# Performance work log

Hardware: AMD Instinct MI355X
Metric: run time of the kernel (lower is better)

## Reference

```python
import jax, jax.numpy as jnp
import numpy as np

DIM = 512
HEADS = 8
WIN = 64


def setup_inputs() -> dict:
    key = jax.random.key(0)
    k1, k2, k3 = jax.random.split(key, 3)
    x = jax.random.normal(k1, (16, 4096, DIM), dtype=jnp.float32)
    Wqkv = jax.random.normal(k2, (DIM, 3 * DIM), dtype=jnp.float32) * 0.02
    Wproj = jax.random.normal(k3, (DIM, DIM), dtype=jnp.float32) * 0.02
    bproj = jnp.zeros((DIM,), dtype=jnp.float32)
    return {"x": x, "Wqkv": Wqkv, "Wproj": Wproj, "bproj": bproj}


def reference(x, Wqkv, Wproj, bproj):
    B0, T0, C = x.shape
    H = HEADS
    hd = C // H
    scale = hd ** -0.5
    # reshape sequence into fixed-size windows: [Bw, W, C]
    xw = x.reshape(-1, WIN, C)
    Bw = xw.shape[0]
    # fused QKV projection (no bias)
    qkv = (xw @ Wqkv).reshape(Bw, WIN, 3, H, hd)
    qkv = jnp.transpose(qkv, (2, 0, 3, 1, 4))  # [3, Bw, H, W, hd]
    q, k, v = qkv[0], qkv[1], qkv[2]
    attn = jnp.einsum('bhqd,bhkd->bhqk', q, k) * scale  # [Bw, H, W, W]
    # causal mask within each window
    mask = jnp.tril(jnp.ones((WIN, WIN), dtype=bool))
    attn = jnp.where(mask, attn, -jnp.inf)
    attn = jax.nn.softmax(attn, axis=-1)
    # faithful to source: second (unconditional) softmax applied on probabilities
    attn = jax.nn.softmax(attn, axis=-1)
    out = jnp.einsum('bhqk,bhkd->bhqd', attn, v)  # [Bw, H, W, hd]
    out = jnp.transpose(out, (0, 2, 1, 3)).reshape(Bw, WIN, C)
    out = out @ Wproj + bproj
    return out.reshape(B0, T0, C)
```

## Files before the change

### kernel.cpp

```cpp
#include <hip/hip_runtime.h>


typedef _Float16 f16x8 __attribute__((ext_vector_type(8)));
typedef _Float16 f16x4 __attribute__((ext_vector_type(4)));
typedef float f32x4 __attribute__((ext_vector_type(4)));

#define MFMA16(a, b, c) __builtin_amdgcn_mfma_f32_16x16x32_f16((a), (b), (c), 0, 0, 0)

__device__ __forceinline__ int swz64(int r, int c) { return r * 64 + (c ^ ((r & 7) << 3)); }
__device__ __forceinline__ int swz512(int r, int c) { return r * 512 + (c ^ ((r & 7) << 3)); }

typedef const __attribute__((address_space(1))) void* gas1_t;
typedef __attribute__((address_space(3))) void* las3_t;

__device__ __forceinline__ void stage16(const _Float16* g, _Float16* lbase, int lane) {
#if __has_builtin(__builtin_amdgcn_global_load_lds)
  __builtin_amdgcn_global_load_lds((gas1_t)(const void*)g, (las3_t)(void*)lbase, 16, 0, 0);
#else
  *(f16x8*)(lbase + lane * 8) = *(const f16x8*)g;
#endif
}

__global__ void prep_weights(const float* __restrict__ Wqkv,
                             const float* __restrict__ Wproj,
                             _Float16* __restrict__ wqkvP,
                             _Float16* __restrict__ wprojP) {
  int idx = blockIdx.x * blockDim.x + threadIdx.x;
  if (idx < 786432) {
    int r16 = idx >> 13;
    int rem = idx & 8191;
    int kt = rem >> 9;
    int lane = (rem >> 3) & 63;
    int e = rem & 7;
    int row = r16 * 16 + (lane & 15);
    int k = kt * 32 + (lane >> 4) * 8 + e;
    float v = Wqkv[k * 1536 + row];
    if (row < 512) v *= 0.125f;
    wqkvP[idx] = (_Float16)v;
  } else {
    int j = idx - 786432;
    int r16 = j >> 13;
    int rem = j & 8191;
    int kt = rem >> 9;
    int lane = (rem >> 3) & 63;
    int e = rem & 7;
    int n = r16 * 16 + (lane & 15);
    int k = kt * 32 + (lane >> 4) * 8 + e;
    wprojP[j] = (_Float16)Wproj[k * 512 + n];
  }
}

__global__ __launch_bounds__(512) void prep_x(const float* __restrict__ x,
                                              _Float16* __restrict__ xP) {
  __shared__ __align__(16) _Float16 sX[64 * 512];
  const int tid = threadIdx.x;
  const float4* xv = (const float4*)(x + (size_t)blockIdx.x * 32768);
#pragma unroll
  for (int it = 0; it < 8; ++it) {
    int g = tid + it * 512;
    int r = g >> 6, c0 = (g & 63) << 3;
    float4 a = xv[(r << 7) + (c0 >> 2)];
    float4 b = xv[(r << 7) + (c0 >> 2) + 1];
    f16x8 hv;
    hv[0] = (_Float16)a.x; hv[1] = (_Float16)a.y;
    hv[2] = (_Float16)a.z; hv[3] = (_Float16)a.w;
    hv[4] = (_Float16)b.x; hv[5] = (_Float16)b.y;
    hv[6] = (_Float16)b.z; hv[7] = (_Float16)b.w;
    *(f16x8*)&sX[swz512(r, c0)] = hv;
  }
  __syncthreads();
  _Float16* dst = xP + (size_t)blockIdx.x * 32768;
#pragma unroll
  for (int it = 0; it < 8; ++it) {
    int c8 = tid + it * 512;
    int rt = c8 >> 10, ks = (c8 >> 6) & 15, ln = c8 & 63;
    int row = rt * 16 + (ln & 15);
    int k0 = ks * 32 + (ln >> 4) * 8;
    f16x8 v = *(const f16x8*)&sX[swz512(row, k0)];
    *(f16x8*)(dst + c8 * 8) = v;
  }
}

template <int MODE>
__global__ __launch_bounds__(512, 2) void gemm2p(
    const _Float16* __restrict__ Afp, const _Float16* __restrict__ Bfp,
    _Float16* __restrict__ dst16, float* __restrict__ out,
    const float* __restrict__ bproj, int rTiles) {
  __shared__ __align__(16) _Float16 sG[2][2][16][512];
  const int tid = threadIdx.x;
  const int wid = tid >> 6;
  const int lane = tid & 63;
  const int lg = lane >> 4, lr = lane & 15;
  const int wr = wid >> 2, wc = wid & 3;
  const int wr8 = wr * 8, wc4 = wc * 4, lane8 = lane * 8;

  const int nwg = gridDim.x;
  const int bid = blockIdx.x;
  const int swz = (bid & 7) * (nwg >> 3) + (bid >> 3);
  const int r0 = (swz % rTiles) * 256, c0 = (swz / rTiles) * 256;

  const _Float16* Abase = Afp + (size_t)(r0 >> 4) * 8192 + lane8;
  const _Float16* Bbase = Bfp + (size_t)(c0 >> 4) * 8192 + lane8;

  const f32x4 zero4 = {0.f, 0.f, 0.f, 0.f};
  f32x4 acc[8][4];
#pragma unroll
  for (int i = 0; i < 8; ++i)
#pragma unroll
    for (int j = 0; j < 4; ++j) acc[i][j] = zero4;

  const int cs = wid * 2;
  auto STAGE = [&](int s, int T) {
    stage16(Abase + (size_t)cs * 8192 + T * 512, &sG[s][0][cs][0], lane);
    stage16(Abase + (size_t)(cs + 1) * 8192 + T * 512, &sG[s][0][cs + 1][0], lane);
    stage16(Bbase + (size_t)cs * 8192 + T * 512, &sG[s][1][cs][0], lane);
    stage16(Bbase + (size_t)(cs + 1) * 8192 + T * 512, &sG[s][1][cs + 1][0], lane);
  };

  STAGE(0, 0);
  int cur = 0;
  for (int t = 0; t < 16; ++t) {
    const int Tn = (t + 1 < 16) ? t + 1 : 15;
    STAGE(cur ^ 1, Tn);
    asm volatile("s_waitcnt vmcnt(4)");
    __builtin_amdgcn_s_barrier();
    __builtin_amdgcn_sched_barrier(0);
    f16x8 a[8], b[4];
#pragma unroll
    for (int mi = 0; mi < 8; ++mi)
      a[mi] = *(const f16x8*)&sG[cur][0][wr8 + mi][lane8];
#pragma unroll
    for (int ni = 0; ni < 4; ++ni)
      b[ni] = *(const f16x8*)&sG[cur][1][wc4 + ni][lane8];
    __builtin_amdgcn_s_setprio(1);
#pragma unroll
    for (int mi = 0; mi < 8; ++mi)
#pragma unroll
      for (int ni = 0; ni < 4; ++ni)
        acc[mi][ni] = MFMA16(a[mi], b[ni], acc[mi][ni]);
    __builtin_amdgcn_s_setprio(0);
    asm volatile("s_waitcnt lgkmcnt(0)");
    __builtin_amdgcn_sched_barrier(0);
    __builtin_amdgcn_s_barrier();
    __builtin_amdgcn_sched_barrier(0);
    cur ^= 1;
  }

  if constexpr (MODE == 0) {
#pragma unroll
    for (int mi = 0; mi < 8; ++mi) {
      int nb = r0 + wr * 128 + mi * 16 + lg * 4;
      int sec = nb >> 9, h = (nb >> 6) & 7, db = nb & 63;
      int coff = (db >> 5) * 512 + (((db >> 3) & 3) * 16) * 8 + (db & 7);
#pragma unroll
      for (int ni = 0; ni < 4; ++ni) {
        int tg = c0 + wc * 64 + ni * 16 + lr;
        int w = tg >> 6, t = tg & 63;
        size_t pos = ((size_t)w * 24 + sec * 8 + h) * 4096 +
                     (size_t)((t >> 4) * 2) * 512 + coff + (t & 15) * 8;
        f16x4 hv;
        hv[0] = (_Float16)acc[mi][ni][0]; hv[1] = (_Float16)acc[mi][ni][1];
        hv[2] = (_Float16)acc[mi][ni][2]; hv[3] = (_Float16)acc[mi][ni][3];
        *(f16x4*)(dst16 + pos) = hv;
      }
    }
  } else if constexpr (MODE == 1) {
#pragma unroll
    for (int mi = 0; mi < 8; ++mi) {
      int tbg = r0 + wr * 128 + mi * 16 + lg * 4;
      int w = tbg >> 6, tb = tbg & 63;
      int coff = (tb >> 5) * 512 + (((tb >> 3) & 3) * 16) * 8 + (tb & 7);
#pragma unroll
      for (int ni = 0; ni < 4; ++ni) {
        int cv = c0 + wc * 64 + ni * 16 + lr;
        int h = cv >> 6, d = cv & 63;
        size_t pos = ((size_t)w * 24 + 16 + h) * 4096 +
                     (size_t)((d >> 4) * 2) * 512 + coff + (d & 15) * 8;
        f16x4 hv;
        hv[0] = (_Float16)acc[mi][ni][0]; hv[1] = (_Float16)acc[mi][ni][1];
        hv[2] = (_Float16)acc[mi][ni][2]; hv[3] = (_Float16)acc[mi][ni][3];
        *(f16x4*)(dst16 + pos) = hv;
      }
    }
  } else {
#pragma unroll
    for (int mi = 0; mi < 8; ++mi) {
      int nb = r0 + wr * 128 + mi * 16 + lg * 4;
      float4 bi = *(const float4*)&bproj[nb];
#pragma unroll
      for (int ni = 0; ni < 4; ++ni) {
        int tg = c0 + wc * 64 + ni * 16 + lr;
        float4 v;
        v.x = acc[mi][ni][0] + bi.x; v.y = acc[mi][ni][1] + bi.y;
        v.z = acc[mi][ni][2] + bi.z; v.w = acc[mi][ni][3] + bi.w;
        *(float4*)&out[(size_t)tg * 512 + nb] = v;
      }
    }
  }
}

__global__ __launch_bounds__(512, 4) void attn_win(
    const _Float16* __restrict__ qkvP, _Float16* __restrict__ hP) {
  __shared__ __align__(16) _Float16 sP[4][4096];
  const int tid = threadIdx.x;
  const int wid = tid >> 6;
  const int lane = tid & 63;
  const int lg = lane >> 4, lr = lane & 15;
  const int hl = wid >> 1, part = wid & 1;
  const int w = blockIdx.x;
  const f32x4 zero4 = {0.f, 0.f, 0.f, 0.f};

  for (int hr = 0; hr < 2; ++hr) {
    const int h = hr * 4 + hl;
    const _Float16* Qb = qkvP + ((size_t)w * 24 + h) * 4096 + lane * 8;
    const _Float16* Kb = qkvP + ((size_t)w * 24 + 8 + h) * 4096 + lane * 8;
    const _Float16* Vb = qkvP + ((size_t)w * 24 + 16 + h) * 4096 + lane * 8;

    f16x8 afq[2][2], bfk[4][2];
#pragma unroll
    for (int rs = 0; rs < 2; ++rs)
#pragma unroll
      for (int dkt = 0; dkt < 2; ++dkt)
        afq[rs][dkt] = *(const f16x8*)(Qb + ((part * 2 + rs) * 2 + dkt) * 512);
#pragma unroll
    for (int nt = 0; nt < 4; ++nt)
#pragma unroll
      for (int dkt = 0; dkt < 2; ++dkt)
        bfk[nt][dkt] = *(const f16x8*)(Kb + (nt * 2 + dkt) * 512);
    f32x4 sacc[2][4];
#pragma unroll
    for (int rs = 0; rs < 2; ++rs)
#pragma unroll
      for (int nt = 0; nt < 4; ++nt) sacc[rs][nt] = zero4;
#pragma unroll
    for (int dkt = 0; dkt < 2; ++dkt)
#pragma unroll
      for (int rs = 0; rs < 2; ++rs)
#pragma unroll
        for (int nt = 0; nt < 4; ++nt)
          sacc[rs][nt] = MFMA16(afq[rs][dkt], bfk[nt][dkt], sacc[rs][nt]);

    f16x8 afv[2][2];
#pragma unroll
    for (int ds = 0; ds < 2; ++ds)
#pragma unroll
      for (int tkt = 0; tkt < 2; ++tkt)
        afv[ds][tkt] = *(const f16x8*)(Vb + ((part * 2 + ds) * 2 + tkt) * 512);

    float p2[2][4][4];
#pragma unroll
    for (int rs = 0; rs < 2; ++rs) {
      const int rsg = part * 2 + rs;
#pragma unroll
      for (int rg = 0; rg < 4; ++rg) {
        int row = rsg * 16 + lg * 4 + rg;
        float m = -1e30f;
#pragma unroll
        for (int nt = 0; nt < 4; ++nt) {
          int col = nt * 16 + lr;
          float v = (col <= row) ? sacc[rs][nt][rg] : -1e30f;
          m = fmaxf(m, v);
        }
#pragma unroll
        for (int off = 8; off >= 1; off >>= 1) m = fmaxf(m, __shfl_xor(m, off));
        float e[4], s1 = 0.f;
#pragma unroll
        for (int nt = 0; nt < 4; ++nt) {
          int col = nt * 16 + lr;
          e[nt] = (col <= row) ? __expf(sacc[rs][nt][rg] - m) : 0.f;
          s1 += e[nt];
        }
#pragma unroll
        for (int off = 8; off >= 1; off >>= 1) s1 += __shfl_xor(s1, off);
        float inv1 = 1.f / s1;
        float e2[4], s2 = 0.f;
#pragma unroll
        for (int nt = 0; nt < 4; ++nt) {
          e2[nt] = __expf(e[nt] * inv1);
          s2 += e2[nt];
        }
#pragma unroll
        for (int off = 8; off >= 1; off >>= 1) s2 += __shfl_xor(s2, off);
        float inv2 = 1.f / s2;
#pragma unroll
        for (int nt = 0; nt < 4; ++nt) p2[rs][nt][rg] = e2[nt] * inv2;
      }
    }

#pragma unroll
    for (int rs = 0; rs < 2; ++rs) {
      const int rsg = part * 2 + rs;
#pragma unroll
      for (int nt = 0; nt < 4; ++nt) {
        int cbase = (rsg * 2 + (nt >> 1)) * 512 +
                    ((((nt * 2) + (lr >> 3)) & 3) * 16 + lg * 4) * 8 + (lr & 7);
#pragma unroll
        for (int rg = 0; rg < 4; ++rg)
          sP[hl][cbase + rg * 8] = (_Float16)p2[rs][nt][rg];
      }
    }
    __syncthreads();

    f32x4 oacc[2][4];
#pragma unroll
    for (int ds = 0; ds < 2; ++ds)
#pragma unroll
      for (int ntq = 0; ntq < 4; ++ntq) oacc[ds][ntq] = zero4;
#pragma unroll
    for (int tkt = 0; tkt < 2; ++tkt) {
      f16x8 bfp[4];
#pragma unroll
      for (int ntq = 0; ntq < 4; ++ntq)
        bfp[ntq] = *(const f16x8*)&sP[hl][(ntq * 2 + tkt) * 512 + lane * 8];
#pragma unroll
      for (int ds = 0; ds < 2; ++ds)
#pragma unroll
        for (int ntq = 0; ntq < 4; ++ntq)
          oacc[ds][ntq] = MFMA16(afv[ds][tkt], bfp[ntq], oacc[ds][ntq]);
    }

#pragma unroll
    for (int ds = 0; ds < 2; ++ds) {
      const int dsg = part * 2 + ds;
      const int e0 = (lg & 1) * 4;
      const int lgt = (dsg * 2 + (lg >> 1)) & 3;
#pragma unroll
      for (int ntq = 0; ntq < 4; ++ntq) {
        size_t pos = ((size_t)(w * 4 + ntq) * 16 + h * 2 + (dsg >> 1)) * 512 +
                     (lgt * 16 + lr) * 8 + e0;
        f16x4 hv;
        hv[0] = (_Float16)oacc[ds][ntq][0]; hv[1] = (_Float16)oacc[ds][ntq][1];
        hv[2] = (_Float16)oacc[ds][ntq][2]; hv[3] = (_Float16)oacc[ds][ntq][3];
        *(f16x4*)(hP + pos) = hv;
      }
    }
    __syncthreads();
  }
}

__global__ __launch_bounds__(512, 2) void attn_fused(
    const float* __restrict__ x, const _Float16* __restrict__ wqkvP,
    const _Float16* __restrict__ wprojP, const float* __restrict__ bproj,
    float* __restrict__ out) {
  __shared__ __align__(16) _Float16 sX[64 * 512];
  __shared__ __align__(16) _Float16 sHeads[4][2][4096];

  const int tid = threadIdx.x;
  const int wid = tid >> 6;
  const int lane = tid & 63;
  const int lg = lane >> 4;
  const int lr = lane & 15;

  _Float16* sQ0 = &sHeads[0][0][0];
  _Float16* sK0 = &sHeads[1][0][0];
  _Float16* sVT0 = &sHeads[2][0][0];
  _Float16* sPO0 = &sHeads[3][0][0];

  const float4* xv = (const float4*)(x + (size_t)blockIdx.x * 32768);
#pragma unroll
  for (int it = 0; it < 8; ++it) {
    int g = tid + it * 512;
    int r = g >> 6, c0 = (g & 63) << 3;
    float4 a = xv[(r << 7) + (c0 >> 2)];
    float4 b = xv[(r << 7) + (c0 >> 2) + 1];
    f16x8 hv;
    hv[0] = (_Float16)a.x; hv[1] = (_Float16)a.y;
    hv[2] = (_Float16)a.z; hv[3] = (_Float16)a.w;
    hv[4] = (_Float16)b.x; hv[5] = (_Float16)b.y;
    hv[6] = (_Float16)b.z; hv[7] = (_Float16)b.w;
    *(f16x8*)&sX[swz512(r, c0)] = hv;
  }
  const f32x4 zero4 = {0.f, 0.f, 0.f, 0.f};
  f32x4 accO[4][4];
#pragma unroll
  for (int i = 0; i < 4; ++i)
#pragma unroll
    for (int j = 0; j < 4; ++j) accO[i][j] = zero4;
  __syncthreads();

  for (int hp = 0; hp < 4; ++hp) {
    int hu[3], su[3], stu[3];
    const _Float16* bp[3];
    f32x4 acc[3][4];
#pragma unroll
    for (int i = 0; i < 3; ++i) {
      int u = wid + 8 * i;
      int hh = u & 1, v2 = u >> 1;
      int sec = v2 % 3, strip = v2 / 3;
      hu[i] = hh; su[i] = sec; stu[i] = strip;
      int r16 = sec * 32 + (hp * 2 + hh) * 4 + strip;
      bp[i] = wqkvP + (size_t)r16 * 8192 + lane * 8;
#pragma unroll
      for (int rt = 0; rt < 4; ++rt) acc[i][rt] = zero4;
    }
    f16x8 bf[3][3];
#pragma unroll
    for (int d = 0; d < 3; ++d)
#pragma unroll
      for (int i = 0; i < 3; ++i) bf[d][i] = *(const f16x8*)(bp[i] + d * 512);
    f16x8 af[2][4];
#pragma unroll
    for (int rt = 0; rt < 4; ++rt)
      af[0][rt] = *(const f16x8*)&sX[swz512(rt * 16 + lr, lg * 8)];
#pragma unroll
    for (int ks = 0; ks < 16; ++ks) {
      if (ks < 15) {
#pragma unroll
        for (int rt = 0; rt < 4; ++rt)
          af[(ks + 1) & 1][rt] =
              *(const f16x8*)&sX[swz512(rt * 16 + lr, (ks + 1) * 32 + lg * 8)];
      }
#pragma unroll
      for (int i = 0; i < 3; ++i)
#pragma unroll
        for (int rt = 0; rt < 4; ++rt)
          acc[i][rt] = MFMA16(af[ks & 1][rt], bf[ks % 3][i], acc[i][rt]);
      if (ks + 3 < 16) {
#pragma unroll
        for (int i = 0; i < 3; ++i)
          bf[ks % 3][i] = *(const f16x8*)(bp[i] + (ks + 3) * 512);
      }
    }
#pragma unroll
    for (int i = 0; i < 3; ++i) {
      int hh = hu[i], sec = su[i], strip = stu[i];
      _Float16* dq = sQ0 + hh * 4096;
      _Float16* dk = sK0 + hh * 4096;
      _Float16* dv = sVT0 + hh * 4096;
#pragma unroll
      for (int rt = 0; rt < 4; ++rt)
#pragma unroll
        for (int rg = 0; rg < 4; ++rg) {
          int row = rt * 16 + lg * 4 + rg;
          int col = strip * 16 + lr;
          _Float16 v = (_Float16)acc[i][rt][rg];
          if (sec == 0) dq[swz64(row, col)] = v;
          else if (sec == 1) dk[swz64(row, col)] = v;
          else dv[swz64(col, row)] = v;
        }
    }
    __syncthreads();
    {
      const int hh = wid >> 2;
      const int rs = wid & 3;
      const _Float16* mQ = sQ0 + hh * 4096;
      const _Float16* mK = sK0 + hh * 4096;
      const _Float16* mV = sVT0 + hh * 4096;
      _Float16* mP = sPO0 + hh * 4096;
      f32x4 sacc[4];
#pragma unroll
      for (int nt = 0; nt < 4; ++nt) sacc[nt] = zero4;
#pragma unroll
      for (int ks = 0; ks < 2; ++ks) {
        f16x8 afq = *(const f16x8*)&mQ[swz64(rs * 16 + lr, ks * 32 + lg * 8)];
#pragma unroll
        for (int nt = 0; nt < 4; ++nt) {
          f16x8 bfk = *(const f16x8*)&mK[swz64(nt * 16 + lr, ks * 32 + lg * 8)];
          sacc[nt] = MFMA16(afq, bfk, sacc[nt]);
        }
      }
      float p2[4][4];
#pragma unroll
      for (int rg = 0; rg < 4; ++rg) {
        int row = rs * 16 + lg * 4 + rg;
        float m = -1e30f;
#pragma unroll
        for (int nt = 0; nt < 4; ++nt) {
          int col = nt * 16 + lr;
          float v = (col <= row) ? sacc[nt][rg] : -1e30f;
          m = fmaxf(m, v);
        }
#pragma unroll
        for (int off = 8; off >= 1; off >>= 1) m = fmaxf(m, __shfl_xor(m, off));
        float e[4], s1 = 0.f;
#pragma unroll
        for (int nt = 0; nt < 4; ++nt) {
          int col = nt * 16 + lr;
          e[nt] = (col <= row) ? __expf(sacc[nt][rg] - m) : 0.f;
          s1 += e[nt];
        }
#pragma unroll
        for (int off = 8; off >= 1; off >>= 1) s1 += __shfl_xor(s1, off);
        float inv1 = 1.f / s1;
        float e2[4], s2 = 0.f;
#pragma unroll
        for (int nt = 0; nt < 4; ++nt) {
          e2[nt] = __expf(e[nt] * inv1);
          s2 += e2[nt];
        }
#pragma unroll
        for (int off = 8; off >= 1; off >>= 1) s2 += __shfl_xor(s2, off);
        float inv2 = 1.f / s2;
#pragma unroll
        for (int nt = 0; nt < 4; ++nt) p2[nt][rg] = e2[nt] * inv2;
      }
#pragma unroll
      for (int nt = 0; nt < 4; ++nt)
#pragma unroll
        for (int rg = 0; rg < 4; ++rg)
          mP[swz64(rs * 16 + lg * 4 + rg, nt * 16 + lr)] = (_Float16)p2[nt][rg];
      asm volatile("" ::: "memory");
      f32x4 oacc[4];
#pragma unroll
      for (int nt = 0; nt < 4; ++nt) oacc[nt] = zero4;
#pragma unroll
      for (int ks = 0; ks < 2; ++ks) {
        f16x8 afp = *(const f16x8*)&mP[swz64(rs * 16 + lr, ks * 32 + lg * 8)];
#pragma unroll
        for (int nt = 0; nt < 4; ++nt) {
          f16x8 bfv = *(const f16x8*)&mV[swz64(nt * 16 + lr, ks * 32 + lg * 8)];
          oacc[nt] = MFMA16(afp, bfv, oacc[nt]);
        }
      }
      asm volatile("" ::: "memory");
#pragma unroll
      for (int nt = 0; nt < 4; ++nt)
#pragma unroll
        for (int rg = 0; rg < 4; ++rg)
          mP[swz64(rs * 16 + lg * 4 + rg, nt * 16 + lr)] = (_Float16)oacc[nt][rg];
    }
    __syncthreads();
    {
      f16x8 bfC[2][4], afC[2][4];
#pragma unroll
      for (int rt = 0; rt < 4; ++rt)
        afC[0][rt] = *(const f16x8*)&sPO0[swz64(rt * 16 + lr, lg * 8)];
#pragma unroll
      for (int nt = 0; nt < 4; ++nt)
        bfC[0][nt] = *(const f16x8*)(wprojP + (size_t)(wid * 4 + nt) * 8192 +
                                     (size_t)(hp * 4) * 512 + lane * 8);
#pragma unroll
      for (int g = 0; g < 4; ++g) {
        if (g < 3) {
          int hn = (g + 1) >> 1, kn = (g + 1) & 1;
#pragma unroll
          for (int rt = 0; rt < 4; ++rt)
            afC[(g + 1) & 1][rt] = *(const f16x8*)&sPO0[hn * 4096 +
                swz64(rt * 16 + lr, kn * 32 + lg * 8)];
#pragma unroll
          for (int nt = 0; nt < 4; ++nt)
            bfC[(g + 1) & 1][nt] =
                *(const f16x8*)(wprojP + (size_t)(wid * 4 + nt) * 8192 +
                                (size_t)(hp * 4 + g + 1) * 512 + lane * 8);
        }
#pragma unroll
        for (int nt = 0; nt < 4; ++nt)
#pragma unroll
          for (int rt = 0; rt < 4; ++rt)
            accO[rt][nt] = MFMA16(afC[g & 1][rt], bfC[g & 1][nt], accO[rt][nt]);
      }
    }
  }
  __syncthreads();
  float bias_r[4];
#pragma unroll
  for (int nt = 0; nt < 4; ++nt) bias_r[nt] = bproj[wid * 64 + nt * 16 + lr];
  float* sEp = (float*)&sHeads[0][0][0];
  size_t base = (size_t)blockIdx.x * 32768;
#pragma unroll
  for (int half = 0; half < 2; ++half) {
#pragma unroll
    for (int rr = 0; rr < 2; ++rr) {
      int rt = half * 2 + rr;
#pragma unroll
      for (int nt = 0; nt < 4; ++nt)
#pragma unroll
        for (int rg = 0; rg < 4; ++rg) {
          int r = rr * 16 + lg * 4 + rg;
          int c = wid * 64 + nt * 16 + lr;
          sEp[r * 512 + (c ^ (((r >> 2) & 1) << 4))] = accO[rt][nt][rg] + bias_r[nt];
        }
    }
    __syncthreads();
#pragma unroll
    for (int j = 0; j < 8; ++j) {
      int f4 = tid + j * 512;
      int r = f4 >> 7;
      int c0 = (f4 & 127) << 2;
      float4 v = *(const float4*)&sEp[r * 512 + (c0 ^ (((r >> 2) & 1) << 4))];
      *(float4*)&out[base + (size_t)(half * 32 + r) * 512 + c0] = v;
    }
    if (half == 0) __syncthreads();
  }
}

extern "C" void kernel_launch(void* const* d_in, const int* in_sizes, int n_in,
                              void* d_out, int out_size, void* d_ws, size_t ws_size,
                              hipStream_t stream) {
  const float* x = (const float*)d_in[0];
  const float* Wqkv = (const float*)d_in[1];
  const float* Wproj = (const float*)d_in[2];
  const float* bproj = (const float*)d_in[3];
  float* out = (float*)d_out;

  const size_t W1 = 786432, W2 = 262144, XN = 33554432;
  const size_t QN = 100663296, HN = 33554432;
  _Float16* wqkvP = (_Float16*)d_ws;
  _Float16* wprojP = wqkvP + W1;
  _Float16* xP = wprojP + W2;
  _Float16* qkvP = xP + XN;
  _Float16* hP = qkvP + QN;
  const size_t NEED = (W1 + W2 + XN + QN + HN) * 2;

  prep_weights<<<dim3(4096), dim3(256), 0, stream>>>(Wqkv, Wproj, wqkvP, wprojP);
  if (ws_size >= NEED) {
    prep_x<<<dim3(1024), dim3(512), 0, stream>>>(x, xP);
    gemm2p<0><<<dim3(1024), dim3(512), 0, stream>>>(wqkvP, xP, qkvP, nullptr, nullptr, 4);
    gemm2p<1><<<dim3(512), dim3(512), 0, stream>>>(xP, wqkvP + (size_t)64 * 8192,
                                                   qkvP, nullptr, nullptr, 256);
    attn_win<<<dim3(1024), dim3(512), 0, stream>>>(qkvP, hP);
    gemm2p<2><<<dim3(512), dim3(512), 0, stream>>>(wprojP, hP, nullptr, out, bproj, 2);
  } else {
    attn_fused<<<dim3(1024), dim3(512), 0, stream>>>(x, wqkvP, wprojP, bproj, out);
  }
}
```

Before: 294.2 us.

## Load GEMM B fragments directly into registers, stage only A through LDS

The GEMM kernel no longer stages the B operand in shared memory. Each wave loads its own B fragments straight from global memory into double-buffered registers, while A keeps LDS double buffering. This halves LDS use and the LDS traffic for B. In exchange, B fragments shared across wave rows are now fetched redundantly from global/L2, register pressure rises, and the loop is fully unrolled.

```diff
diff --git a/kernel.cpp b/kernel.cpp
--- a/kernel.cpp
+++ b/kernel.cpp
@@ -7,8 +7,8 @@
 
 #define MFMA16(a, b, c) __builtin_amdgcn_mfma_f32_16x16x32_f16((a), (b), (c), 0, 0, 0)
 
+__device__ __forceinline__ int swz512(int r, int c) { return r * 512 + (c ^ ((r & 7) << 3)); }
 __device__ __forceinline__ int swz64(int r, int c) { return r * 64 + (c ^ ((r & 7) << 3)); }
-__device__ __forceinline__ int swz512(int r, int c) { return r * 512 + (c ^ ((r & 7) << 3)); }
 
 typedef const __attribute__((address_space(1))) void* gas1_t;
 typedef __attribute__((address_space(3))) void* las3_t;
@@ -82,17 +82,18 @@
 }
 
 template <int MODE>
-__global__ __launch_bounds__(512, 2) void gemm2p(
+__global__ __launch_bounds__(512, 2) void gemmd(
     const _Float16* __restrict__ Afp, const _Float16* __restrict__ Bfp,
     _Float16* __restrict__ dst16, float* __restrict__ out,
     const float* __restrict__ bproj, int rTiles) {
-  __shared__ __align__(16) _Float16 sG[2][2][16][512];
+  __shared__ __align__(16) _Float16 sA[2][16][512];
   const int tid = threadIdx.x;
   const int wid = tid >> 6;
   const int lane = tid & 63;
   const int lg = lane >> 4, lr = lane & 15;
   const int wr = wid >> 2, wc = wid & 3;
   const int wr8 = wr * 8, wc4 = wc * 4, lane8 = lane * 8;
+  const int cs = wid * 2;
 
   const int nwg = gridDim.x;
   const int bid = blockIdx.x;
@@ -100,7 +101,12 @@
   const int r0 = (swz % rTiles) * 256, c0 = (swz / rTiles) * 256;
 
   const _Float16* Abase = Afp + (size_t)(r0 >> 4) * 8192 + lane8;
-  const _Float16* Bbase = Bfp + (size_t)(c0 >> 4) * 8192 + lane8;
+  const _Float16* Bfrag = Bfp + (size_t)((c0 >> 4) + wc4) * 8192 + lane8;
+
+  auto ASTAGE = [&](int s, int T) {
+    stage16(Abase + (size_t)cs * 8192 + T * 512, &sA[s][cs][0], lane);
+    stage16(Abase + (size_t)(cs + 1) * 8192 + T * 512, &sA[s][cs + 1][0], lane);
+  };
 
   const f32x4 zero4 = {0.f, 0.f, 0.f, 0.f};
   f32x4 acc[8][4];
@@ -109,41 +115,53 @@
 #pragma unroll
     for (int j = 0; j < 4; ++j) acc[i][j] = zero4;
 
-  const int cs = wid * 2;
-  auto STAGE = [&](int s, int T) {
-    stage16(Abase + (size_t)cs * 8192 + T * 512, &sG[s][0][cs][0], lane);
-    stage16(Abase + (size_t)(cs + 1) * 8192 + T * 512, &sG[s][0][cs + 1][0], lane);
-    stage16(Bbase + (size_t)cs * 8192 + T * 512, &sG[s][1][cs][0], lane);
-    stage16(Bbase + (size_t)(cs + 1) * 8192 + T * 512, &sG[s][1][cs + 1][0], lane);
-  };
-
-  STAGE(0, 0);
-  int cur = 0;
+  f16x8 bA[4], bB[4];
+#pragma unroll
+  for (int ni = 0; ni < 4; ++ni)
+    bA[ni] = *(const f16x8*)(Bfrag + (size_t)ni * 8192);
+  ASTAGE(0, 0);
+
+#pragma unroll
   for (int t = 0; t < 16; ++t) {
+    const int s = t & 1, sn = s ^ 1;
     const int Tn = (t + 1 < 16) ? t + 1 : 15;
-    STAGE(cur ^ 1, Tn);
-    asm volatile("s_waitcnt vmcnt(4)");
+    if ((t & 1) == 0) {
+#pragma unroll
+      for (int ni = 0; ni < 4; ++ni)
+        bB[ni] = *(const f16x8*)(Bfrag + (size_t)ni * 8192 + Tn * 512);
+    } else {
+#pragma unroll
+      for (int ni = 0; ni < 4; ++ni)
+        bA[ni] = *(const f16x8*)(Bfrag + (size_t)ni * 8192 + Tn * 512);
+    }
+    ASTAGE(sn, Tn);
+    __builtin_amdgcn_sched_barrier(0);
+    asm volatile("s_waitcnt vmcnt(6)");
     __builtin_amdgcn_s_barrier();
     __builtin_amdgcn_sched_barrier(0);
-    f16x8 a[8], b[4];
+    f16x8 a[8];
 #pragma unroll
     for (int mi = 0; mi < 8; ++mi)
-      a[mi] = *(const f16x8*)&sG[cur][0][wr8 + mi][lane8];
-#pragma unroll
-    for (int ni = 0; ni < 4; ++ni)
-      b[ni] = *(const f16x8*)&sG[cur][1][wc4 + ni][lane8];
+      a[mi] = *(const f16x8*)&sA[s][wr8 + mi][lane8];
     __builtin_amdgcn_s_setprio(1);
-#pragma unroll
-    for (int mi = 0; mi < 8; ++mi)
-#pragma unroll
-      for (int ni = 0; ni < 4; ++ni)
-        acc[mi][ni] = MFMA16(a[mi], b[ni], acc[mi][ni]);
+    if ((t & 1) == 0) {
+#pragma unroll
+      for (int mi = 0; mi < 8; ++mi)
+#pragma unroll
+        for (int ni = 0; ni < 4; ++ni)
+          acc[mi][ni] = MFMA16(a[mi], bA[ni], acc[mi][ni]);
+    } else {
+#pragma unroll
+      for (int mi = 0; mi < 8; ++mi)
+#pragma unroll
+        for (int ni = 0; ni < 4; ++ni)
+          acc[mi][ni] = MFMA16(a[mi], bB[ni], acc[mi][ni]);
+    }
     __builtin_amdgcn_s_setprio(0);
     asm volatile("s_waitcnt lgkmcnt(0)");
     __builtin_amdgcn_sched_barrier(0);
     __builtin_amdgcn_s_barrier();
     __builtin_amdgcn_sched_barrier(0);
-    cur ^= 1;
   }
 
   if constexpr (MODE == 0) {
@@ -605,11 +623,11 @@
   prep_weights<<<dim3(4096), dim3(256), 0, stream>>>(Wqkv, Wproj, wqkvP, wprojP);
   if (ws_size >= NEED) {
     prep_x<<<dim3(1024), dim3(512), 0, stream>>>(x, xP);
-    gemm2p<0><<<dim3(1024), dim3(512), 0, stream>>>(wqkvP, xP, qkvP, nullptr, nullptr, 4);
-    gemm2p<1><<<dim3(512), dim3(512), 0, stream>>>(xP, wqkvP + (size_t)64 * 8192,
-                                                   qkvP, nullptr, nullptr, 256);
+    gemmd<0><<<dim3(1024), dim3(512), 0, stream>>>(wqkvP, xP, qkvP, nullptr, nullptr, 4);
+    gemmd<1><<<dim3(512), dim3(512), 0, stream>>>(xP, wqkvP + (size_t)64 * 8192,
+                                                  qkvP, nullptr, nullptr, 256);
     attn_win<<<dim3(1024), dim3(512), 0, stream>>>(qkvP, hP);
-    gemm2p<2><<<dim3(512), dim3(512), 0, stream>>>(wprojP, hP, nullptr, out, bproj, 2);
+    gemmd<2><<<dim3(512), dim3(512), 0, stream>>>(wprojP, hP, nullptr, out, bproj, 2);
   } else {
     attn_fused<<<dim3(1024), dim3(512), 0, stream>>>(x, wqkvP, wprojP, bproj, out);
   }
```

Result: slower. 300.6 us (+2.2%).

## Merge QKV GEMMs into one launch and fuse attention with output projection

Applied to the files above, without the earlier changes.

The separate Q/K and V GEMM launches become a single 1536-block GEMM whose epilogue branches by output section and writes V with scalar transposed stores. The attention kernel now also performs the output projection per window: each head pair's output goes to LDS and is multiplied by Wproj fragments read from global memory, accumulating in registers. This removes the intermediate head buffer round trip through HBM and one kernel launch. In exchange, V is written with 2-byte scalar stores, Wproj is reread by every window block, and the attention kernel needs more registers at lower occupancy.

```diff
diff --git a/kernel.cpp b/kernel.cpp
--- a/kernel.cpp
+++ b/kernel.cpp
@@ -7,8 +7,8 @@
 
 #define MFMA16(a, b, c) __builtin_amdgcn_mfma_f32_16x16x32_f16((a), (b), (c), 0, 0, 0)
 
+__device__ __forceinline__ int swz512(int r, int c) { return r * 512 + (c ^ ((r & 7) << 3)); }
 __device__ __forceinline__ int swz64(int r, int c) { return r * 64 + (c ^ ((r & 7) << 3)); }
-__device__ __forceinline__ int swz512(int r, int c) { return r * 512 + (c ^ ((r & 7) << 3)); }
 
 typedef const __attribute__((address_space(1))) void* gas1_t;
 typedef __attribute__((address_space(3))) void* las3_t;
@@ -81,11 +81,9 @@
   }
 }
 
-template <int MODE>
-__global__ __launch_bounds__(512, 2) void gemm2p(
+__global__ __launch_bounds__(512, 2) void gemmQKV(
     const _Float16* __restrict__ Afp, const _Float16* __restrict__ Bfp,
-    _Float16* __restrict__ dst16, float* __restrict__ out,
-    const float* __restrict__ bproj, int rTiles) {
+    _Float16* __restrict__ dst16) {
   __shared__ __align__(16) _Float16 sG[2][2][16][512];
   const int tid = threadIdx.x;
   const int wid = tid >> 6;
@@ -93,29 +91,29 @@
   const int lg = lane >> 4, lr = lane & 15;
   const int wr = wid >> 2, wc = wid & 3;
   const int wr8 = wr * 8, wc4 = wc * 4, lane8 = lane * 8;
+  const int cs = wid * 2;
 
   const int nwg = gridDim.x;
   const int bid = blockIdx.x;
   const int swz = (bid & 7) * (nwg >> 3) + (bid >> 3);
-  const int r0 = (swz % rTiles) * 256, c0 = (swz / rTiles) * 256;
+  const int r0 = (swz % 6) * 256, c0 = (swz / 6) * 256;
 
   const _Float16* Abase = Afp + (size_t)(r0 >> 4) * 8192 + lane8;
   const _Float16* Bbase = Bfp + (size_t)(c0 >> 4) * 8192 + lane8;
 
-  const f32x4 zero4 = {0.f, 0.f, 0.f, 0.f};
-  f32x4 acc[8][4];
-#pragma unroll
-  for (int i = 0; i < 8; ++i)
-#pragma unroll
-    for (int j = 0; j < 4; ++j) acc[i][j] = zero4;
-
-  const int cs = wid * 2;
   auto STAGE = [&](int s, int T) {
     stage16(Abase + (size_t)cs * 8192 + T * 512, &sG[s][0][cs][0], lane);
     stage16(Abase + (size_t)(cs + 1) * 8192 + T * 512, &sG[s][0][cs + 1][0], lane);
     stage16(Bbase + (size_t)cs * 8192 + T * 512, &sG[s][1][cs][0], lane);
     stage16(Bbase + (size_t)(cs + 1) * 8192 + T * 512, &sG[s][1][cs + 1][0], lane);
   };
+
+  const f32x4 zero4 = {0.f, 0.f, 0.f, 0.f};
+  f32x4 acc[8][4];
+#pragma unroll
+  for (int i = 0; i < 8; ++i)
+#pragma unroll
+    for (int j = 0; j < 4; ++j) acc[i][j] = zero4;
 
   STAGE(0, 0);
   int cur = 0;
@@ -146,10 +144,10 @@
     cur ^= 1;
   }
 
-  if constexpr (MODE == 0) {
-#pragma unroll
-    for (int mi = 0; mi < 8; ++mi) {
-      int nb = r0 + wr * 128 + mi * 16 + lg * 4;
+#pragma unroll
+  for (int mi = 0; mi < 8; ++mi) {
+    int nb = r0 + wr * 128 + mi * 16 + lg * 4;
+    if (nb < 1024) {
       int sec = nb >> 9, h = (nb >> 6) & 7, db = nb & 63;
       int coff = (db >> 5) * 512 + (((db >> 3) & 3) * 16) * 8 + (db & 7);
 #pragma unroll
@@ -163,102 +161,71 @@
         hv[2] = (_Float16)acc[mi][ni][2]; hv[3] = (_Float16)acc[mi][ni][3];
         *(f16x4*)(dst16 + pos) = hv;
       }
-    }
-  } else if constexpr (MODE == 1) {
-#pragma unroll
-    for (int mi = 0; mi < 8; ++mi) {
-      int tbg = r0 + wr * 128 + mi * 16 + lg * 4;
-      int w = tbg >> 6, tb = tbg & 63;
-      int coff = (tb >> 5) * 512 + (((tb >> 3) & 3) * 16) * 8 + (tb & 7);
-#pragma unroll
-      for (int ni = 0; ni < 4; ++ni) {
-        int cv = c0 + wc * 64 + ni * 16 + lr;
-        int h = cv >> 6, d = cv & 63;
-        size_t pos = ((size_t)w * 24 + 16 + h) * 4096 +
-                     (size_t)((d >> 4) * 2) * 512 + coff + (d & 15) * 8;
-        f16x4 hv;
-        hv[0] = (_Float16)acc[mi][ni][0]; hv[1] = (_Float16)acc[mi][ni][1];
-        hv[2] = (_Float16)acc[mi][ni][2]; hv[3] = (_Float16)acc[mi][ni][3];
-        *(f16x4*)(dst16 + pos) = hv;
-      }
-    }
-  } else {
-#pragma unroll
-    for (int mi = 0; mi < 8; ++mi) {
-      int nb = r0 + wr * 128 + mi * 16 + lg * 4;
-      float4 bi = *(const float4*)&bproj[nb];
+    } else {
+      int h = (nb >> 6) & 7, db = nb & 63;
 #pragma unroll
       for (int ni = 0; ni < 4; ++ni) {
         int tg = c0 + wc * 64 + ni * 16 + lr;
-        float4 v;
-        v.x = acc[mi][ni][0] + bi.x; v.y = acc[mi][ni][1] + bi.y;
-        v.z = acc[mi][ni][2] + bi.z; v.w = acc[mi][ni][3] + bi.w;
-        *(float4*)&out[(size_t)tg * 512 + nb] = v;
-      }
-    }
-  }
-}
-
-__global__ __launch_bounds__(512, 4) void attn_win(
-    const _Float16* __restrict__ qkvP, _Float16* __restrict__ hP) {
-  __shared__ __align__(16) _Float16 sP[4][4096];
+        int w = tg >> 6, t = tg & 63;
+        size_t base2 = ((size_t)w * 24 + 16 + h) * 4096 +
+                       (size_t)((db >> 4) * 2 + (t >> 5)) * 512 +
+                       (((t >> 3) & 3) * 16) * 8 + (t & 7);
+#pragma unroll
+        for (int rg = 0; rg < 4; ++rg)
+          dst16[base2 + ((db & 15) + rg) * 8] = (_Float16)acc[mi][ni][rg];
+      }
+    }
+  }
+}
+
+__global__ __launch_bounds__(512, 2) void attn_proj(
+    const _Float16* __restrict__ qkvP, const _Float16* __restrict__ wprojP,
+    const float* __restrict__ bproj, float* __restrict__ out) {
+  __shared__ __align__(16) _Float16 sPO[2][4096];
   const int tid = threadIdx.x;
   const int wid = tid >> 6;
   const int lane = tid & 63;
   const int lg = lane >> 4, lr = lane & 15;
-  const int hl = wid >> 1, part = wid & 1;
   const int w = blockIdx.x;
   const f32x4 zero4 = {0.f, 0.f, 0.f, 0.f};
 
-  for (int hr = 0; hr < 2; ++hr) {
-    const int h = hr * 4 + hl;
-    const _Float16* Qb = qkvP + ((size_t)w * 24 + h) * 4096 + lane * 8;
-    const _Float16* Kb = qkvP + ((size_t)w * 24 + 8 + h) * 4096 + lane * 8;
-    const _Float16* Vb = qkvP + ((size_t)w * 24 + 16 + h) * 4096 + lane * 8;
-
-    f16x8 afq[2][2], bfk[4][2];
-#pragma unroll
-    for (int rs = 0; rs < 2; ++rs)
-#pragma unroll
-      for (int dkt = 0; dkt < 2; ++dkt)
-        afq[rs][dkt] = *(const f16x8*)(Qb + ((part * 2 + rs) * 2 + dkt) * 512);
-#pragma unroll
-    for (int nt = 0; nt < 4; ++nt)
-#pragma unroll
-      for (int dkt = 0; dkt < 2; ++dkt)
-        bfk[nt][dkt] = *(const f16x8*)(Kb + (nt * 2 + dkt) * 512);
-    f32x4 sacc[2][4];
-#pragma unroll
-    for (int rs = 0; rs < 2; ++rs)
-#pragma unroll
-      for (int nt = 0; nt < 4; ++nt) sacc[rs][nt] = zero4;
-#pragma unroll
-    for (int dkt = 0; dkt < 2; ++dkt)
-#pragma unroll
-      for (int rs = 0; rs < 2; ++rs)
-#pragma unroll
-        for (int nt = 0; nt < 4; ++nt)
-          sacc[rs][nt] = MFMA16(afq[rs][dkt], bfk[nt][dkt], sacc[rs][nt]);
-
-    f16x8 afv[2][2];
-#pragma unroll
-    for (int ds = 0; ds < 2; ++ds)
-#pragma unroll
-      for (int tkt = 0; tkt < 2; ++tkt)
-        afv[ds][tkt] = *(const f16x8*)(Vb + ((part * 2 + ds) * 2 + tkt) * 512);
-
-    float p2[2][4][4];
-#pragma unroll
-    for (int rs = 0; rs < 2; ++rs) {
-      const int rsg = part * 2 + rs;
+  f32x4 accO[4][4];
+#pragma unroll
+  for (int i = 0; i < 4; ++i)
+#pragma unroll
+    for (int j = 0; j < 4; ++j) accO[i][j] = zero4;
+
+  for (int hp = 0; hp < 4; ++hp) {
+    {
+      const int hh = wid >> 2;
+      const int rs = wid & 3;
+      const int h = hp * 2 + hh;
+      const _Float16* Qb = qkvP + ((size_t)w * 24 + h) * 4096 + lane * 8;
+      const _Float16* Kb = qkvP + ((size_t)w * 24 + 8 + h) * 4096 + lane * 8;
+      const _Float16* Vb = qkvP + ((size_t)w * 24 + 16 + h) * 4096 + lane * 8;
+      _Float16* mP = &sPO[hh][0];
+
+      f32x4 sacc[4];
+#pragma unroll
+      for (int nt = 0; nt < 4; ++nt) sacc[nt] = zero4;
+#pragma unroll
+      for (int dkt = 0; dkt < 2; ++dkt) {
+        f16x8 afq = *(const f16x8*)(Qb + (rs * 2 + dkt) * 512);
+#pragma unroll
+        for (int nt = 0; nt < 4; ++nt) {
+          f16x8 bfk = *(const f16x8*)(Kb + (nt * 2 + dkt) * 512);
+          sacc[nt] = MFMA16(afq, bfk, sacc[nt]);
+        }
+      }
+      float p2[4][4];
 #pragma unroll
       for (int rg = 0; rg < 4; ++rg) {
-        int row = rsg * 16 + lg * 4 + rg;
+        int row = rs * 16 + lg * 4 + rg;
         float m = -1e30f;
 #pragma unroll
         for (int nt = 0; nt < 4; ++nt) {
           int col = nt * 16 + lr;
-          float v = (col <= row) ? sacc[rs][nt][rg] : -1e30f;
+          float v = (col <= row) ? sacc[nt][rg] : -1e30f;
           m = fmaxf(m, v);
         }
 #pragma unroll
@@ -267,7 +234,7 @@
 #pragma unroll
         for (int nt = 0; nt < 4; ++nt) {
           int col = nt * 16 + lr;
-          e[nt] = (col <= row) ? __expf(sacc[rs][nt][rg] - m) : 0.f;
+          e[nt] = (col <= row) ? __expf(sacc[nt][rg] - m) : 0.f;
           s1 += e[nt];
         }
 #pragma unroll
@@ -283,58 +250,66 @@
         for (int off = 8; off >= 1; off >>= 1) s2 += __shfl_xor(s2, off);
         float inv2 = 1.f / s2;
 #pragma unroll
-        for (int nt = 0; nt < 4; ++nt) p2[rs][nt][rg] = e2[nt] * inv2;
-      }
-    }
-
-#pragma unroll
-    for (int rs = 0; rs < 2; ++rs) {
-      const int rsg = part * 2 + rs;
+        for (int nt = 0; nt < 4; ++nt) p2[nt][rg] = e2[nt] * inv2;
+      }
+#pragma unroll
+      for (int nt = 0; nt < 4; ++nt)
+#pragma unroll
+        for (int rg = 0; rg < 4; ++rg)
+          mP[swz64(rs * 16 + lg * 4 + rg, nt * 16 + lr)] = (_Float16)p2[nt][rg];
+      asm volatile("" ::: "memory");
+      f32x4 oacc[4];
+#pragma unroll
+      for (int nt = 0; nt < 4; ++nt) oacc[nt] = zero4;
+#pragma unroll
+      for (int tkt = 0; tkt < 2; ++tkt) {
+        f16x8 afp = *(const f16x8*)&mP[swz64(rs * 16 + lr, tkt * 32 + lg * 8)];
+#pragma unroll
+        for (int nt = 0; nt < 4; ++nt) {
+          f16x8 bfv = *(const f16x8*)(Vb + (nt * 2 + tkt) * 512);
+          oacc[nt] = MFMA16(afp, bfv, oacc[nt]);
+        }
+      }
+      asm volatile("" ::: "memory");
+#pragma unroll
+      for (int nt = 0; nt < 4; ++nt)
+#pragma unroll
+        for (int rg = 0; rg < 4; ++rg)
+          mP[swz64(rs * 16 + lg * 4 + rg, nt * 16 + lr)] = (_Float16)oacc[nt][rg];
+    }
+    __syncthreads();
+
+#pragma unroll
+    for (int ks = 0; ks < 4; ++ks) {
+      const int hh = ks >> 1, d0 = (ks & 1) * 32 + lg * 8;
+      f16x8 bf[4];
+#pragma unroll
+      for (int tt = 0; tt < 4; ++tt)
+        bf[tt] = *(const f16x8*)&sPO[hh][swz64(tt * 16 + lr, d0)];
 #pragma unroll
       for (int nt = 0; nt < 4; ++nt) {
-        int cbase = (rsg * 2 + (nt >> 1)) * 512 +
-                    ((((nt * 2) + (lr >> 3)) & 3) * 16 + lg * 4) * 8 + (lr & 7);
-#pragma unroll
-        for (int rg = 0; rg < 4; ++rg)
-          sP[hl][cbase + rg * 8] = (_Float16)p2[rs][nt][rg];
+        f16x8 aw = *(const f16x8*)(wprojP + (size_t)(wid * 4 + nt) * 8192 +
+                                   (size_t)(hp * 4 + ks) * 512 + lane * 8);
+#pragma unroll
+        for (int tt = 0; tt < 4; ++tt)
+          accO[nt][tt] = MFMA16(aw, bf[tt], accO[nt][tt]);
       }
     }
     __syncthreads();
-
-    f32x4 oacc[2][4];
-#pragma unroll
-    for (int ds = 0; ds < 2; ++ds)
-#pragma unroll
-      for (int ntq = 0; ntq < 4; ++ntq) oacc[ds][ntq] = zero4;
-#pragma unroll
-    for (int tkt = 0; tkt < 2; ++tkt) {
-      f16x8 bfp[4];
-#pragma unroll
-      for (int ntq = 0; ntq < 4; ++ntq)
-        bfp[ntq] = *(const f16x8*)&sP[hl][(ntq * 2 + tkt) * 512 + lane * 8];
-#pragma unroll
-      for (int ds = 0; ds < 2; ++ds)
-#pragma unroll
-        for (int ntq = 0; ntq < 4; ++ntq)
-          oacc[ds][ntq] = MFMA16(afv[ds][tkt], bfp[ntq], oacc[ds][ntq]);
-    }
-
-#pragma unroll
-    for (int ds = 0; ds < 2; ++ds) {
-      const int dsg = part * 2 + ds;
-      const int e0 = (lg & 1) * 4;
-      const int lgt = (dsg * 2 + (lg >> 1)) & 3;
-#pragma unroll
-      for (int ntq = 0; ntq < 4; ++ntq) {
-        size_t pos = ((size_t)(w * 4 + ntq) * 16 + h * 2 + (dsg >> 1)) * 512 +
-                     (lgt * 16 + lr) * 8 + e0;
-        f16x4 hv;
-        hv[0] = (_Float16)oacc[ds][ntq][0]; hv[1] = (_Float16)oacc[ds][ntq][1];
-        hv[2] = (_Float16)oacc[ds][ntq][2]; hv[3] = (_Float16)oacc[ds][ntq][3];
-        *(f16x4*)(hP + pos) = hv;
-      }
-    }
-    __syncthreads();
+  }
+
+#pragma unroll
+  for (int nt = 0; nt < 4; ++nt) {
+    int nb = wid * 64 + nt * 16 + lg * 4;
+    float4 bi = *(const float4*)&bproj[nb];
+#pragma unroll
+    for (int tt = 0; tt < 4; ++tt) {
+      int tok = tt * 16 + lr;
+      float4 v;
+      v.x = accO[nt][tt][0] + bi.x; v.y = accO[nt][tt][1] + bi.y;
+      v.z = accO[nt][tt][2] + bi.z; v.w = accO[nt][tt][3] + bi.w;
+      *(float4*)&out[((size_t)w * 64 + tok) * 512 + nb] = v;
+    }
   }
 }
 
@@ -593,23 +568,18 @@
   const float* bproj = (const float*)d_in[3];
   float* out = (float*)d_out;
 
-  const size_t W1 = 786432, W2 = 262144, XN = 33554432;
-  const size_t QN = 100663296, HN = 33554432;
+  const size_t W1 = 786432, W2 = 262144, XN = 33554432, QN = 100663296;
   _Float16* wqkvP = (_Float16*)d_ws;
   _Float16* wprojP = wqkvP + W1;
   _Float16* xP = wprojP + W2;
   _Float16* qkvP = xP + XN;
-  _Float16* hP = qkvP + QN;
-  const size_t NEED = (W1 + W2 + XN + QN + HN) * 2;
+  const size_t NEED = (W1 + W2 + XN + QN) * 2;
 
   prep_weights<<<dim3(4096), dim3(256), 0, stream>>>(Wqkv, Wproj, wqkvP, wprojP);
   if (ws_size >= NEED) {
     prep_x<<<dim3(1024), dim3(512), 0, stream>>>(x, xP);
-    gemm2p<0><<<dim3(1024), dim3(512), 0, stream>>>(wqkvP, xP, qkvP, nullptr, nullptr, 4);
-    gemm2p<1><<<dim3(512), dim3(512), 0, stream>>>(xP, wqkvP + (size_t)64 * 8192,
-                                                   qkvP, nullptr, nullptr, 256);
-    attn_win<<<dim3(1024), dim3(512), 0, stream>>>(qkvP, hP);
-    gemm2p<2><<<dim3(512), dim3(512), 0, stream>>>(wprojP, hP, nullptr, out, bproj, 2);
+    gemmQKV<<<dim3(1536), dim3(512), 0, stream>>>(wqkvP, xP, qkvP);
+    attn_proj<<<dim3(1024), dim3(512), 0, stream>>>(qkvP, wprojP, bproj, out);
   } else {
     attn_fused<<<dim3(1024), dim3(512), 0, stream>>>(x, wqkvP, wprojP, bproj, out);
   }
```

After: 301.2 us. 1.02x slower.

## Shrink GEMM tiles to 128x128 and fold V projection into QKV GEMM

Applied to the files above, without the earlier changes.

Replaces the 256x256-tile, 512-thread GEMM with a 128x128-tile, 256-thread variant and raises the block counts. The separate V-projection GEMM (MODE 1) is dropped. V is now computed by the weight-major QKV GEMM, with a scalar scatter epilogue that writes V in its transposed layout. Smaller tiles give more blocks and better occupancy, and removing a launch cuts overhead. The costs are lower per-tile data reuse and uncoalesced 2-byte stores for the V section.

```diff
diff --git a/kernel.cpp b/kernel.cpp
--- a/kernel.cpp
+++ b/kernel.cpp
@@ -7,8 +7,8 @@
 
 #define MFMA16(a, b, c) __builtin_amdgcn_mfma_f32_16x16x32_f16((a), (b), (c), 0, 0, 0)
 
+__device__ __forceinline__ int swz512(int r, int c) { return r * 512 + (c ^ ((r & 7) << 3)); }
 __device__ __forceinline__ int swz64(int r, int c) { return r * 64 + (c ^ ((r & 7) << 3)); }
-__device__ __forceinline__ int swz512(int r, int c) { return r * 512 + (c ^ ((r & 7) << 3)); }
 
 typedef const __attribute__((address_space(1))) void* gas1_t;
 typedef __attribute__((address_space(3))) void* las3_t;
@@ -82,40 +82,40 @@
 }
 
 template <int MODE>
-__global__ __launch_bounds__(512, 2) void gemm2p(
+__global__ __launch_bounds__(256) void gemm128(
     const _Float16* __restrict__ Afp, const _Float16* __restrict__ Bfp,
     _Float16* __restrict__ dst16, float* __restrict__ out,
     const float* __restrict__ bproj, int rTiles) {
-  __shared__ __align__(16) _Float16 sG[2][2][16][512];
+  __shared__ __align__(16) _Float16 sG[2][2][8][512];
   const int tid = threadIdx.x;
   const int wid = tid >> 6;
   const int lane = tid & 63;
   const int lg = lane >> 4, lr = lane & 15;
-  const int wr = wid >> 2, wc = wid & 3;
-  const int wr8 = wr * 8, wc4 = wc * 4, lane8 = lane * 8;
+  const int wr = wid >> 1, wc = wid & 1;
+  const int wr4 = wr * 4, wc4 = wc * 4, lane8 = lane * 8;
+  const int cs = wid * 2;
 
   const int nwg = gridDim.x;
   const int bid = blockIdx.x;
   const int swz = (bid & 7) * (nwg >> 3) + (bid >> 3);
-  const int r0 = (swz % rTiles) * 256, c0 = (swz / rTiles) * 256;
+  const int r0 = (swz % rTiles) * 128, c0 = (swz / rTiles) * 128;
 
   const _Float16* Abase = Afp + (size_t)(r0 >> 4) * 8192 + lane8;
   const _Float16* Bbase = Bfp + (size_t)(c0 >> 4) * 8192 + lane8;
 
-  const f32x4 zero4 = {0.f, 0.f, 0.f, 0.f};
-  f32x4 acc[8][4];
-#pragma unroll
-  for (int i = 0; i < 8; ++i)
-#pragma unroll
-    for (int j = 0; j < 4; ++j) acc[i][j] = zero4;
-
-  const int cs = wid * 2;
   auto STAGE = [&](int s, int T) {
     stage16(Abase + (size_t)cs * 8192 + T * 512, &sG[s][0][cs][0], lane);
     stage16(Abase + (size_t)(cs + 1) * 8192 + T * 512, &sG[s][0][cs + 1][0], lane);
     stage16(Bbase + (size_t)cs * 8192 + T * 512, &sG[s][1][cs][0], lane);
     stage16(Bbase + (size_t)(cs + 1) * 8192 + T * 512, &sG[s][1][cs + 1][0], lane);
   };
+
+  const f32x4 zero4 = {0.f, 0.f, 0.f, 0.f};
+  f32x4 acc[4][4];
+#pragma unroll
+  for (int i = 0; i < 4; ++i)
+#pragma unroll
+    for (int j = 0; j < 4; ++j) acc[i][j] = zero4;
 
   STAGE(0, 0);
   int cur = 0;
@@ -125,16 +125,16 @@
     asm volatile("s_waitcnt vmcnt(4)");
     __builtin_amdgcn_s_barrier();
     __builtin_amdgcn_sched_barrier(0);
-    f16x8 a[8], b[4];
-#pragma unroll
-    for (int mi = 0; mi < 8; ++mi)
-      a[mi] = *(const f16x8*)&sG[cur][0][wr8 + mi][lane8];
+    f16x8 a[4], b[4];
+#pragma unroll
+    for (int mi = 0; mi < 4; ++mi)
+      a[mi] = *(const f16x8*)&sG[cur][0][wr4 + mi][lane8];
 #pragma unroll
     for (int ni = 0; ni < 4; ++ni)
       b[ni] = *(const f16x8*)&sG[cur][1][wc4 + ni][lane8];
     __builtin_amdgcn_s_setprio(1);
 #pragma unroll
-    for (int mi = 0; mi < 8; ++mi)
+    for (int mi = 0; mi < 4; ++mi)
 #pragma unroll
       for (int ni = 0; ni < 4; ++ni)
         acc[mi][ni] = MFMA16(a[mi], b[ni], acc[mi][ni]);
@@ -148,44 +148,41 @@
 
   if constexpr (MODE == 0) {
 #pragma unroll
-    for (int mi = 0; mi < 8; ++mi) {
-      int nb = r0 + wr * 128 + mi * 16 + lg * 4;
-      int sec = nb >> 9, h = (nb >> 6) & 7, db = nb & 63;
-      int coff = (db >> 5) * 512 + (((db >> 3) & 3) * 16) * 8 + (db & 7);
-#pragma unroll
-      for (int ni = 0; ni < 4; ++ni) {
-        int tg = c0 + wc * 64 + ni * 16 + lr;
-        int w = tg >> 6, t = tg & 63;
-        size_t pos = ((size_t)w * 24 + sec * 8 + h) * 4096 +
-                     (size_t)((t >> 4) * 2) * 512 + coff + (t & 15) * 8;
-        f16x4 hv;
-        hv[0] = (_Float16)acc[mi][ni][0]; hv[1] = (_Float16)acc[mi][ni][1];
-        hv[2] = (_Float16)acc[mi][ni][2]; hv[3] = (_Float16)acc[mi][ni][3];
-        *(f16x4*)(dst16 + pos) = hv;
-      }
-    }
-  } else if constexpr (MODE == 1) {
-#pragma unroll
-    for (int mi = 0; mi < 8; ++mi) {
-      int tbg = r0 + wr * 128 + mi * 16 + lg * 4;
-      int w = tbg >> 6, tb = tbg & 63;
-      int coff = (tb >> 5) * 512 + (((tb >> 3) & 3) * 16) * 8 + (tb & 7);
-#pragma unroll
-      for (int ni = 0; ni < 4; ++ni) {
-        int cv = c0 + wc * 64 + ni * 16 + lr;
-        int h = cv >> 6, d = cv & 63;
-        size_t pos = ((size_t)w * 24 + 16 + h) * 4096 +
-                     (size_t)((d >> 4) * 2) * 512 + coff + (d & 15) * 8;
-        f16x4 hv;
-        hv[0] = (_Float16)acc[mi][ni][0]; hv[1] = (_Float16)acc[mi][ni][1];
-        hv[2] = (_Float16)acc[mi][ni][2]; hv[3] = (_Float16)acc[mi][ni][3];
-        *(f16x4*)(dst16 + pos) = hv;
+    for (int mi = 0; mi < 4; ++mi) {
+      int nb = r0 + wr * 64 + mi * 16 + lg * 4;
+      if (nb < 1024) {
+        int sec = nb >> 9, h = (nb >> 6) & 7, db = nb & 63;
+        int coff = (db >> 5) * 512 + (((db >> 3) & 3) * 16) * 8 + (db & 7);
+#pragma unroll
+        for (int ni = 0; ni < 4; ++ni) {
+          int tg = c0 + wc * 64 + ni * 16 + lr;
+          int w = tg >> 6, t = tg & 63;
+          size_t pos = ((size_t)w * 24 + sec * 8 + h) * 4096 +
+                       (size_t)((t >> 4) * 2) * 512 + coff + (t & 15) * 8;
+          f16x4 hv;
+          hv[0] = (_Float16)acc[mi][ni][0]; hv[1] = (_Float16)acc[mi][ni][1];
+          hv[2] = (_Float16)acc[mi][ni][2]; hv[3] = (_Float16)acc[mi][ni][3];
+          *(f16x4*)(dst16 + pos) = hv;
+        }
+      } else {
+        int h = (nb >> 6) & 7, db = nb & 63;
+#pragma unroll
+        for (int ni = 0; ni < 4; ++ni) {
+          int tg = c0 + wc * 64 + ni * 16 + lr;
+          int w = tg >> 6, t = tg & 63;
+          size_t base2 = ((size_t)w * 24 + 16 + h) * 4096 +
+                         (size_t)((db >> 4) * 2 + (t >> 5)) * 512 +
+                         (((t >> 3) & 3) * 16) * 8 + (t & 7);
+#pragma unroll
+          for (int rg = 0; rg < 4; ++rg)
+            dst16[base2 + ((db & 15) + rg) * 8] = (_Float16)acc[mi][ni][rg];
+        }
       }
     }
   } else {
 #pragma unroll
-    for (int mi = 0; mi < 8; ++mi) {
-      int nb = r0 + wr * 128 + mi * 16 + lg * 4;
+    for (int mi = 0; mi < 4; ++mi) {
+      int nb = r0 + wr * 64 + mi * 16 + lg * 4;
       float4 bi = *(const float4*)&bproj[nb];
 #pragma unroll
       for (int ni = 0; ni < 4; ++ni) {
@@ -605,11 +602,11 @@
   prep_weights<<<dim3(4096), dim3(256), 0, stream>>>(Wqkv, Wproj, wqkvP, wprojP);
   if (ws_size >= NEED) {
     prep_x<<<dim3(1024), dim3(512), 0, stream>>>(x, xP);
-    gemm2p<0><<<dim3(1024), dim3(512), 0, stream>>>(wqkvP, xP, qkvP, nullptr, nullptr, 4);
-    gemm2p<1><<<dim3(512), dim3(512), 0, stream>>>(xP, wqkvP + (size_t)64 * 8192,
-                                                   qkvP, nullptr, nullptr, 256);
+    gemm128<0><<<dim3(6144), dim3(256), 0, stream>>>(wqkvP, xP, qkvP, nullptr,
+                                                     nullptr, 12);
     attn_win<<<dim3(1024), dim3(512), 0, stream>>>(qkvP, hP);
-    gemm2p<2><<<dim3(512), dim3(512), 0, stream>>>(wprojP, hP, nullptr, out, bproj, 2);
+    gemm128<2><<<dim3(2048), dim3(256), 0, stream>>>(wprojP, hP, nullptr, out,
+                                                     bproj, 4);
   } else {
     attn_fused<<<dim3(1024), dim3(512), 0, stream>>>(x, wqkvP, wprojP, bproj, out);
   }
```

Measured after the change: 294.7 us. No clear change (+0.2%).
